# Performance work log

Measured on AMD Instinct MI355X. Metric: run time of the kernel, lower is better.

The kernel has to match this reference:

```python
import jax, jax.numpy as jnp
import numpy as np

# CogForge GroupedQueryAttention (prefill path): GQA + RoPE + sliding-window+global-token mask
B, T, DM = 2, 2048, 768
H, HKV, DH = 12, 4, 64          # d_head = d_model // n_heads
GROUPS = H // HKV               # kv_groups = 3
WIN, GLB = 512, 64              # window_size, global_tokens
THETA = 10000.0


def _rotate_half(x):
    half = x.shape[-1] // 2
    return jnp.concatenate([-x[..., half:], x[..., :half]], axis=-1)


def _rope_cos_sin(seq_len, dim, dtype):
    inv_freq = 1.0 / (THETA ** (jnp.arange(0, dim, 2, dtype=jnp.float32) / dim))
    t = jnp.arange(seq_len, dtype=jnp.float32)
    freqs = jnp.outer(t, inv_freq)                      # [T, DH/2]
    emb = jnp.concatenate([freqs, freqs], axis=-1)      # [T, DH]
    return jnp.cos(emb).astype(dtype)[None, None], jnp.sin(emb).astype(dtype)[None, None]


def _sparse_mask(seq_len):
    # allowed(i,j) = causal AND (within window OR j is a global token)
    i = jnp.arange(seq_len)[:, None]
    j = jnp.arange(seq_len)[None, :]
    allowed = (j <= i) & (((i - j) < WIN) | (j < GLB))
    return jnp.where(allowed, 0.0, -jnp.inf).astype(jnp.float32)  # [T, T]


def setup_inputs() -> dict:
    key = jax.random.key(0)
    kx, kq, kk, kv, ko = jax.random.split(key, 5)
    x = jax.random.normal(kx, (B, T, DM), jnp.float32)
    wq = jax.random.normal(kq, (DM, H * DH), jnp.float32) * 0.02
    wk = jax.random.normal(kk, (DM, HKV * DH), jnp.float32) * 0.02
    wv = jax.random.normal(kv, (DM, HKV * DH), jnp.float32) * 0.02
    wo = jax.random.normal(ko, (H * DH, DM), jnp.float32) * 0.02
    return {"x": x, "wq": wq, "wk": wk, "wv": wv, "wo": wo}


def reference(x, wq, wk, wv, wo):
    # projections -> [B, heads, T, DH]
    q = (x @ wq).reshape(B, T, H, DH).transpose(0, 2, 1, 3)
    k = (x @ wk).reshape(B, T, HKV, DH).transpose(0, 2, 1, 3)
    v = (x @ wv).reshape(B, T, HKV, DH).transpose(0, 2, 1, 3)

    cos, sin = _rope_cos_sin(T, DH, x.dtype)            # [1,1,T,DH]
    q = q * cos + _rotate_half(q) * sin
    k = k * cos + _rotate_half(k) * sin

    # expand kv heads to match query heads (GQA)
    k = jnp.repeat(k, GROUPS, axis=1)                   # [B,H,T,DH]
    v = jnp.repeat(v, GROUPS, axis=1)

    scale = 1.0 / jnp.sqrt(jnp.asarray(DH, x.dtype))
    scores = jnp.einsum('bhtd,bhsd->bhts', q, k) * scale
    scores = scores + _sparse_mask(T)[None, None]
    weights = jax.nn.softmax(scores, axis=-1)           # attn_dropout = 0.0

    out = jnp.einsum('bhts,bhsd->bhtd', weights, v)
    out = out.transpose(0, 2, 1, 3).reshape(B, T, H * DH)
    return out @ wo
```

## Files before the change

### kernel.cpp

```cpp
#include <hip/hip_runtime.h>
#include <hip/hip_bf16.h>


typedef __attribute__((ext_vector_type(8))) short bf16x8;
typedef __attribute__((ext_vector_type(4))) float f32x4;
typedef __attribute__((ext_vector_type(4))) unsigned short u16x4;

#define MFMA __builtin_amdgcn_mfma_f32_16x16x32_bf16

constexpr int BB = 2, TT = 2048, DM = 768, HH = 12, HKV = 4, DH = 64;
constexpr int WIN = 512, GLB = 64;
constexpr float SC2 = 0.18033688011112042f;

__device__ __forceinline__ unsigned short f2b(float f) {
    union { float f; unsigned int u; } v; v.f = f;
    unsigned int r = v.u + 0x7fffu + ((v.u >> 16) & 1u);
    return (unsigned short)(r >> 16);
}

#define GLOAD_LDS(gp, lp)                                                      \
    __builtin_amdgcn_global_load_lds(                                          \
        (const __attribute__((address_space(1))) void*)(gp),                   \
        (__attribute__((address_space(3))) void*)(lp), 16, 0, 0)

__global__ __launch_bounds__(256) void k_pre(const float* __restrict__ x,
                                             unsigned short* __restrict__ xb,
                                             float2* __restrict__ rope,
                                             const float* __restrict__ wq,
                                             const float* __restrict__ wk,
                                             const float* __restrict__ wv,
                                             const float* __restrict__ wo,
                                             unsigned short* __restrict__ wqT,
                                             unsigned short* __restrict__ wkT,
                                             unsigned short* __restrict__ wvT,
                                             unsigned short* __restrict__ woT) {
    __shared__ float t[32][33];
    int bid = blockIdx.x, tid = threadIdx.x;
    if (bid < 3072) {
        int i = bid * 256 + tid;
        float4 v = ((const float4*)x)[i];
        u16x4 o; o.x = f2b(v.x); o.y = f2b(v.y); o.z = f2b(v.z); o.w = f2b(v.w);
        ((u16x4*)xb)[i] = o;
        return;
    }
    if (bid < 3328) {
        int i = (bid - 3072) * 256 + tid;
        int tt = i >> 5, p = i & 31;
        float inv = exp2f(-(float)p * (13.287712379549449f / 32.0f));
        float ang = (float)tt * inv;
        rope[i] = make_float2(cosf(ang), sinf(ang));
        return;
    }
    int wb = bid - 3328;
    const float* src; unsigned short* dst; int N, tile;
    if (wb < 576)      { src = wq; dst = wqT; N = 768; tile = wb; }
    else if (wb < 768) { src = wk; dst = wkT; N = 256; tile = wb - 576; }
    else if (wb < 960) { src = wv; dst = wvT; N = 256; tile = wb - 768; }
    else               { src = wo; dst = woT; N = 768; tile = wb - 960; }
    int ntiles = N / 32;
    int k0 = (tile / ntiles) * 32, n0 = (tile % ntiles) * 32;
    int tx = tid & 31, ty = tid >> 5;
    #pragma unroll
    for (int e = 0; e < 4; ++e) {
        int r = ty + e * 8;
        t[r][tx] = src[(size_t)(k0 + r) * N + n0 + tx];
    }
    __syncthreads();
    #pragma unroll
    for (int e = 0; e < 4; ++e) {
        int r = ty + e * 8;
        dst[(size_t)(n0 + r) * DM + k0 + tx] = f2b(t[tx][r]);
    }
}

__global__ __launch_bounds__(256) void k_qkv(const unsigned short* __restrict__ xb,
                                             const unsigned short* __restrict__ wqT,
                                             const unsigned short* __restrict__ wkT,
                                             const unsigned short* __restrict__ wvT,
                                             unsigned short* __restrict__ qb,
                                             unsigned short* __restrict__ kb,
                                             unsigned short* __restrict__ vtb,
                                             const float2* __restrict__ rope) {
    __shared__ __align__(16) unsigned short Ab[2][128 * 64];
    __shared__ __align__(16) unsigned short Bb[2][64 * 64];
    const int tid = threadIdx.x;
    const int wave = tid >> 6, lane = tid & 63;
    const int quad = lane >> 4, col = lane & 15;
    const int y = blockIdx.y;
    int mode, hl;
    const unsigned short* Bt;
    if (y < 12)      { mode = 0; hl = y;      Bt = wqT + (size_t)hl * 64 * DM; }
    else if (y < 16) { mode = 1; hl = y - 12; Bt = wkT + (size_t)hl * 64 * DM; }
    else             { mode = 2; hl = y - 16; Bt = wvT + (size_t)hl * 64 * DM; }
    const int m0b = blockIdx.x * 128;

    const int rg = lane >> 3;
    const int cg = (lane & 7) ^ rg;
    const int ck = col & 7;

    f32x4 acc[2][4];
    #pragma unroll
    for (int rt = 0; rt < 2; ++rt)
        #pragma unroll
        for (int j = 0; j < 4; ++j) acc[rt][j] = f32x4{0.f, 0.f, 0.f, 0.f};

    auto stage = [&](int buf, int k) {
        #pragma unroll
        for (int m = 0; m < 4; ++m) {
            int g = wave * 4 + m;
            GLOAD_LDS(xb + (size_t)(m0b + g * 8 + rg) * DM + k + cg * 8,
                      &Ab[buf][g * 512]);
        }
        #pragma unroll
        for (int m = 0; m < 2; ++m) {
            int g = wave * 2 + m;
            GLOAD_LDS(Bt + (size_t)(g * 8 + rg) * DM + k + cg * 8,
                      &Bb[buf][g * 512]);
        }
    };

    stage(0, 0);
    __syncthreads();

    const int arow0 = (wave * 32 + col) * 64;
    const int arow1 = (wave * 32 + 16 + col) * 64;

    for (int t = 0; t < 12; ++t) {
        const int buf = t & 1;
        if (t < 11) stage(buf ^ 1, (t + 1) * 64);
        __builtin_amdgcn_s_setprio(1);
        #pragma unroll
        for (int ks = 0; ks < 2; ++ks) {
            const int p = ((ks * 4 + quad) ^ ck) * 8;
            bf16x8 a0 = *(const bf16x8*)&Ab[buf][arow0 + p];
            bf16x8 a1 = *(const bf16x8*)&Ab[buf][arow1 + p];
            #pragma unroll
            for (int j = 0; j < 4; ++j) {
                bf16x8 b = *(const bf16x8*)&Bb[buf][(j * 16 + col) * 64 + p];
                acc[0][j] = MFMA(a0, b, acc[0][j], 0, 0, 0);
                acc[1][j] = MFMA(a1, b, acc[1][j], 0, 0, 0);
            }
        }
        __builtin_amdgcn_s_setprio(0);
        __syncthreads();
    }

    if (mode == 2) {
        int b = m0b >> 11;
        #pragma unroll
        for (int j = 0; j < 4; ++j)
            #pragma unroll
            for (int rt = 0; rt < 2; ++rt)
                #pragma unroll
                for (int r = 0; r < 4; ++r) {
                    int m = m0b + wave * 32 + rt * 16 + quad * 4 + r;
                    int t = m & (TT - 1);
                    int d = j * 16 + col;
                    vtb[((size_t)(b * HKV + hl) * DH + d) * TT + t] = f2b(acc[rt][j][r]);
                }
        return;
    }
    int nheads = (mode == 0) ? HH : HKV;
    unsigned short* ob = (mode == 0) ? qb : kb;
    #pragma unroll
    for (int rt = 0; rt < 2; ++rt)
        #pragma unroll
        for (int r = 0; r < 4; ++r) {
            int m = m0b + wave * 32 + rt * 16 + quad * 4 + r;
            int t = m & (TT - 1);
            int b = m >> 11;
            float2 cs0 = rope[t * 32 + col];
            float2 cs1 = rope[t * 32 + 16 + col];
            float v0 = acc[rt][0][r], v1 = acc[rt][1][r], v2 = acc[rt][2][r], v3 = acc[rt][3][r];
            unsigned short* dst = ob + ((size_t)(b * nheads + hl) * TT + t) * DH + col;
            dst[0]  = f2b(v0 * cs0.x - v2 * cs0.y);
            dst[16] = f2b(v1 * cs1.x - v3 * cs1.y);
            dst[32] = f2b(v2 * cs0.x + v0 * cs0.y);
            dst[48] = f2b(v3 * cs1.x + v1 * cs1.y);
        }
}

__global__ __launch_bounds__(256) void k_out(const unsigned short* __restrict__ ao,
                                             const unsigned short* __restrict__ woT,
                                             float* __restrict__ out) {
    __shared__ __align__(16) unsigned short Ab[2][128 * 64];
    __shared__ __align__(16) unsigned short Bb[2][64 * 64];
    const int tid = threadIdx.x;
    const int wave = tid >> 6, lane = tid & 63;
    const int quad = lane >> 4, col = lane & 15;
    const int m0b = blockIdx.x * 128;
    const int n0 = blockIdx.y * 64;

    const int rg = lane >> 3;
    const int cg = (lane & 7) ^ rg;
    const int ck = col & 7;

    f32x4 acc[2][4];
    #pragma unroll
    for (int rt = 0; rt < 2; ++rt)
        #pragma unroll
        for (int j = 0; j < 4; ++j) acc[rt][j] = f32x4{0.f, 0.f, 0.f, 0.f};

    auto stage = [&](int buf, int k) {
        #pragma unroll
        for (int m = 0; m < 4; ++m) {
            int g = wave * 4 + m;
            GLOAD_LDS(ao + (size_t)(m0b + g * 8 + rg) * DM + k + cg * 8,
                      &Ab[buf][g * 512]);
        }
        #pragma unroll
        for (int m = 0; m < 2; ++m) {
            int g = wave * 2 + m;
            GLOAD_LDS(woT + (size_t)(n0 + g * 8 + rg) * DM + k + cg * 8,
                      &Bb[buf][g * 512]);
        }
    };

    stage(0, 0);
    __syncthreads();

    const int arow0 = (wave * 32 + col) * 64;
    const int arow1 = (wave * 32 + 16 + col) * 64;

    for (int t = 0; t < 12; ++t) {
        const int buf = t & 1;
        if (t < 11) stage(buf ^ 1, (t + 1) * 64);
        __builtin_amdgcn_s_setprio(1);
        #pragma unroll
        for (int ks = 0; ks < 2; ++ks) {
            const int p = ((ks * 4 + quad) ^ ck) * 8;
            bf16x8 a0 = *(const bf16x8*)&Ab[buf][arow0 + p];
            bf16x8 a1 = *(const bf16x8*)&Ab[buf][arow1 + p];
            #pragma unroll
            for (int j = 0; j < 4; ++j) {
                bf16x8 b = *(const bf16x8*)&Bb[buf][(j * 16 + col) * 64 + p];
                acc[0][j] = MFMA(a0, b, acc[0][j], 0, 0, 0);
                acc[1][j] = MFMA(a1, b, acc[1][j], 0, 0, 0);
            }
        }
        __builtin_amdgcn_s_setprio(0);
        __syncthreads();
    }

    #pragma unroll
    for (int rt = 0; rt < 2; ++rt)
        #pragma unroll
        for (int j = 0; j < 4; ++j)
            #pragma unroll
            for (int r = 0; r < 4; ++r) {
                int m = m0b + wave * 32 + rt * 16 + quad * 4 + r;
                out[(size_t)m * DM + n0 + j * 16 + col] = acc[rt][j][r];
            }
}

__global__ __launch_bounds__(256) void k_attn(const unsigned short* __restrict__ Q,
                                              const unsigned short* __restrict__ K,
                                              const unsigned short* __restrict__ Vt,
                                              unsigned short* __restrict__ AO) {
    __shared__ __align__(16) unsigned short kbuf[2][64 * 64];
    __shared__ __align__(16) unsigned short vbuf[2][64 * 64];
    const int lane = threadIdx.x & 63;
    const int wave = threadIdx.x >> 6;
    const int quad = lane >> 4, col = lane & 15;
    const int lbid = (blockIdx.x & 7) * 96 + (blockIdx.x >> 3);
    const int qb = lbid & 31, bh = lbid >> 5;
    const int h = bh % HH, b = bh / HH;
    const int hkv = h / 3;
    const int i0 = qb * 64 + wave * 16;
    const int irow = i0 + col;

    const unsigned short* qbase = Q + ((size_t)(b * HH + h) * TT + irow) * DH + quad * 8;
    const bf16x8 qf0 = *(const bf16x8*)qbase;
    const bf16x8 qf1 = *(const bf16x8*)(qbase + 32);
    const unsigned short* kbase = K + (size_t)(b * HKV + hkv) * TT * DH;
    const unsigned short* vbase = Vt + (size_t)(b * HKV + hkv) * DH * TT;

    float m_run = -1e30f, l_lane = 0.f;
    f32x4 accO[4];
    #pragma unroll
    for (int dt = 0; dt < 4; ++dt) accO[dt] = f32x4{0.f, 0.f, 0.f, 0.f};

    int jw0 = (qb * 64 - WIN + 1) & ~63; if (jw0 < 64) jw0 = 64;
    const int jlast = qb * 64;
    const int nt = 1 + ((jlast >= 64) ? (((jlast - jw0) >> 6) + 1) : 0);
    auto j0_of = [&](int t) { return (t == 0) ? 0 : (jw0 + ((t - 1) << 6)); };

    const int srow = wave * 16 + (lane >> 3);
    const int sk = (lane >> 3) & 7;
    const int sq = (lane & 7) ^ sk;
    const int ck = col & 7;

    const int L0 = ((((quad * 2) & 3) << 4) | col) << 2;
    const int L1 = ((((quad * 2 + 1) & 3) << 4) | col) << 2;
    const bool hiq = quad >= 2;

    uint4 g0, g1, g2, g3;
    auto stage_load = [&](int j0) {
        const unsigned short* ks = kbase + (size_t)(j0 + srow) * DH + sq * 8;
        const unsigned short* vs = vbase + (size_t)srow * TT + j0 + sq * 8;
        g0 = *(const uint4*)ks;
        g1 = *(const uint4*)(ks + 8 * DH);
        g2 = *(const uint4*)vs;
        g3 = *(const uint4*)(vs + 8 * TT);
    };
    auto stage_write = [&](int bb) {
        unsigned short* kd = &kbuf[bb][srow * 64 + (lane & 7) * 8];
        unsigned short* vd = &vbuf[bb][srow * 64 + (lane & 7) * 8];
        *(uint4*)kd = g0;
        *(uint4*)(kd + 8 * 64) = g1;
        *(uint4*)vd = g2;
        *(uint4*)(vd + 8 * 64) = g3;
    };

    stage_load(0);
    stage_write(0);
    __syncthreads();

    for (int t = 0; t < nt; ++t) {
        const int bb = t & 1;
        const bool more = (t + 1) < nt;
        if (more) stage_load(j0_of(t + 1));

        const int j0 = j0_of(t);
        const int mode = (t == 0) ? ((i0 < 64) ? 1 : 0)
                       : (((j0 + 63 > i0) || (j0 <= i0 + 15 - WIN)) ? 2 : 0);

        f32x4 sT[4];
        #pragma unroll
        for (int f = 0; f < 4; ++f) sT[f] = f32x4{0.f, 0.f, 0.f, 0.f};
        __builtin_amdgcn_s_setprio(1);
        #pragma unroll
        for (int f = 0; f < 4; ++f) {
            bf16x8 k0 = *(const bf16x8*)&kbuf[bb][(f * 16 + col) * 64 + (quad ^ ck) * 8];
            bf16x8 k1 = *(const bf16x8*)&kbuf[bb][(f * 16 + col) * 64 + ((4 + quad) ^ ck) * 8];
            sT[f] = MFMA(k0, qf0, sT[f], 0, 0, 0);
            sT[f] = MFMA(k1, qf1, sT[f], 0, 0, 0);
        }
        __builtin_amdgcn_s_setprio(0);

        const int dq = irow - j0 - quad * 4;
        if (mode == 1) {
            #pragma unroll
            for (int f = 0; f < 4; ++f)
                #pragma unroll
                for (int r = 0; r < 4; ++r)
                    if (dq - f * 16 - r < 0) sT[f][r] = -3e30f;
        } else if (mode == 2) {
            #pragma unroll
            for (int f = 0; f < 4; ++f)
                #pragma unroll
                for (int r = 0; r < 4; ++r)
                    if ((unsigned)(dq - f * 16 - r) >= (unsigned)WIN) sT[f][r] = -3e30f;
        }

        float mx = -3e30f;
        #pragma unroll
        for (int f = 0; f < 4; ++f)
            #pragma unroll
            for (int r = 0; r < 4; ++r) mx = fmaxf(mx, sT[f][r]);

        if (!__all(mx <= m_run + 44.f)) {
            float rm = fmaxf(mx, __shfl_xor(mx, 16));
            rm = fmaxf(rm, __shfl_xor(rm, 32));
            float mn = fmaxf(m_run, rm);
            float corr = exp2f((m_run - mn) * SC2);
            m_run = mn;
            l_lane *= corr;
            #pragma unroll
            for (int dt = 0; dt < 4; ++dt)
                #pragma unroll
                for (int r = 0; r < 4; ++r) accO[dt][r] *= corr;
        }

        const float mbase = m_run * SC2;
        unsigned int pk[4][2];
        float ps = 0.f;
        #pragma unroll
        for (int f = 0; f < 4; ++f) {
            float p0 = exp2f(__builtin_fmaf(sT[f][0], SC2, -mbase));
            float p1 = exp2f(__builtin_fmaf(sT[f][1], SC2, -mbase));
            float p2 = exp2f(__builtin_fmaf(sT[f][2], SC2, -mbase));
            float p3 = exp2f(__builtin_fmaf(sT[f][3], SC2, -mbase));
            ps += (p0 + p1) + (p2 + p3);
            asm("v_cvt_pk_bf16_f32 %0, %1, %2" : "=v"(pk[f][0]) : "v"(p0), "v"(p1));
            asm("v_cvt_pk_bf16_f32 %0, %1, %2" : "=v"(pk[f][1]) : "v"(p2), "v"(p3));
        }
        l_lane += ps;

        bf16x8 vf[8];
        #pragma unroll
        for (int js = 0; js < 2; ++js)
            #pragma unroll
            for (int dt = 0; dt < 4; ++dt)
                vf[js * 4 + dt] = *(const bf16x8*)
                    &vbuf[bb][(dt * 16 + col) * 64 + ((js * 4 + quad) ^ ck) * 8];

        #pragma unroll
        for (int js = 0; js < 2; ++js) {
            int fa = 2 * js, fb = 2 * js + 1;
            unsigned int a0 = __builtin_amdgcn_ds_bpermute(L0, pk[fa][0]);
            unsigned int a1 = __builtin_amdgcn_ds_bpermute(L0, pk[fa][1]);
            unsigned int a2 = __builtin_amdgcn_ds_bpermute(L1, pk[fa][0]);
            unsigned int a3 = __builtin_amdgcn_ds_bpermute(L1, pk[fa][1]);
            unsigned int b0 = __builtin_amdgcn_ds_bpermute(L0, pk[fb][0]);
            unsigned int b1 = __builtin_amdgcn_ds_bpermute(L0, pk[fb][1]);
            unsigned int b2 = __builtin_amdgcn_ds_bpermute(L1, pk[fb][0]);
            unsigned int b3 = __builtin_amdgcn_ds_bpermute(L1, pk[fb][1]);
            union { bf16x8 v; unsigned int u[4]; } pb;
            pb.u[0] = hiq ? b0 : a0;
            pb.u[1] = hiq ? b1 : a1;
            pb.u[2] = hiq ? b2 : a2;
            pb.u[3] = hiq ? b3 : a3;
            __builtin_amdgcn_s_setprio(1);
            #pragma unroll
            for (int dt = 0; dt < 4; ++dt)
                accO[dt] = MFMA(vf[js * 4 + dt], pb.v, accO[dt], 0, 0, 0);
            __builtin_amdgcn_s_setprio(0);
        }

        if (more) stage_write(bb ^ 1);
        __syncthreads();
    }

    float lr = l_lane;
    lr += __shfl_xor(lr, 16);
    lr += __shfl_xor(lr, 32);
    const float inv = 1.0f / lr;

    unsigned short* dst = AO + ((size_t)b * TT + irow) * DM + h * DH + quad * 4;
    #pragma unroll
    for (int dt = 0; dt < 4; ++dt) {
        u16x4 o;
        o.x = f2b(accO[dt][0] * inv);
        o.y = f2b(accO[dt][1] * inv);
        o.z = f2b(accO[dt][2] * inv);
        o.w = f2b(accO[dt][3] * inv);
        *(u16x4*)(dst + dt * 16) = o;
    }
}

extern "C" void kernel_launch(void* const* d_in, const int* in_sizes, int n_in,
                              void* d_out, int out_size, void* d_ws, size_t ws_size,
                              hipStream_t stream) {
    const float* x  = (const float*)d_in[0];
    const float* wq = (const float*)d_in[1];
    const float* wk = (const float*)d_in[2];
    const float* wv = (const float*)d_in[3];
    const float* wo = (const float*)d_in[4];
    float* out = (float*)d_out;

    char* ws = (char*)d_ws;
    size_t off = 0;
    auto alloc = [&](size_t bytes) -> void* {
        void* p = ws + off;
        off += (bytes + 255) & ~(size_t)255;
        return p;
    };
    const int M = BB * TT;
    unsigned short* xb  = (unsigned short*)alloc((size_t)M * DM * 2);
    unsigned short* wqT = (unsigned short*)alloc((size_t)DM * DM * 2);
    unsigned short* wkT = (unsigned short*)alloc((size_t)(HKV * DH) * DM * 2);
    unsigned short* wvT = (unsigned short*)alloc((size_t)(HKV * DH) * DM * 2);
    unsigned short* woT = (unsigned short*)alloc((size_t)DM * DM * 2);
    unsigned short* qb  = (unsigned short*)alloc((size_t)BB * HH * TT * DH * 2);
    unsigned short* kb  = (unsigned short*)alloc((size_t)BB * HKV * TT * DH * 2);
    unsigned short* vtb = (unsigned short*)alloc((size_t)BB * HKV * DH * TT * 2);
    unsigned short* ao  = (unsigned short*)alloc((size_t)M * DM * 2);
    float2* rope        = (float2*)alloc((size_t)TT * 32 * sizeof(float2));

    k_pre<<<4864, 256, 0, stream>>>(x, xb, rope, wq, wk, wv, wo, wqT, wkT, wvT, woT);
    k_qkv<<<dim3(M / 128, 20), 256, 0, stream>>>(xb, wqT, wkT, wvT, qb, kb, vtb, rope);
    k_attn<<<768, 256, 0, stream>>>(qb, kb, vtb, ao);
    k_out<<<dim3(M / 128, 12), 256, 0, stream>>>(ao, woT, out);
}
```

Measured before the change: 61.36 us.

## Give each attention wave two query tiles and stage K/V with direct-to-LDS loads

The attention kernel now runs 2 waves per block instead of 4, and each wave handles 32 query rows as two 16-row tiles. Each K and V fragment read from LDS feeds the MFMAs of both tiles, with separate softmax state per tile. K/V tile staging switches from register loads plus LDS stores to global_load_lds direct writes, issued at the top of the iteration into the other buffer. This halves LDS fragment reads per query row and removes the register round trip in staging, at the cost of more VGPRs per wave and fewer waves per block, which may lower latency hiding.

```diff
diff --git a/kernel.cpp b/kernel.cpp
--- a/kernel.cpp
+++ b/kernel.cpp
@@ -253,7 +253,7 @@
             }
 }
 
-__global__ __launch_bounds__(256) void k_attn(const unsigned short* __restrict__ Q,
+__global__ __launch_bounds__(128) void k_attn(const unsigned short* __restrict__ Q,
                                               const unsigned short* __restrict__ K,
                                               const unsigned short* __restrict__ Vt,
                                               unsigned short* __restrict__ AO) {
@@ -266,126 +266,138 @@
     const int qb = lbid & 31, bh = lbid >> 5;
     const int h = bh % HH, b = bh / HH;
     const int hkv = h / 3;
-    const int i0 = qb * 64 + wave * 16;
-    const int irow = i0 + col;
-
-    const unsigned short* qbase = Q + ((size_t)(b * HH + h) * TT + irow) * DH + quad * 8;
-    const bf16x8 qf0 = *(const bf16x8*)qbase;
-    const bf16x8 qf1 = *(const bf16x8*)(qbase + 32);
+    const int i0 = qb * 64 + wave * 32;
+    const int ir0 = i0 + col, ir1 = i0 + 16 + col;
+
+    const unsigned short* qp0 = Q + ((size_t)(b * HH + h) * TT + ir0) * DH + quad * 8;
+    const unsigned short* qp1 = Q + ((size_t)(b * HH + h) * TT + ir1) * DH + quad * 8;
+    const bf16x8 qA0 = *(const bf16x8*)qp0;
+    const bf16x8 qA1 = *(const bf16x8*)(qp0 + 32);
+    const bf16x8 qB0 = *(const bf16x8*)qp1;
+    const bf16x8 qB1 = *(const bf16x8*)(qp1 + 32);
     const unsigned short* kbase = K + (size_t)(b * HKV + hkv) * TT * DH;
     const unsigned short* vbase = Vt + (size_t)(b * HKV + hkv) * DH * TT;
 
-    float m_run = -1e30f, l_lane = 0.f;
-    f32x4 accO[4];
-    #pragma unroll
-    for (int dt = 0; dt < 4; ++dt) accO[dt] = f32x4{0.f, 0.f, 0.f, 0.f};
+    float mA = -1e30f, lA = 0.f, mB = -1e30f, lB = 0.f;
+    f32x4 oA[4], oB[4];
+    #pragma unroll
+    for (int dt = 0; dt < 4; ++dt) { oA[dt] = f32x4{0.f,0.f,0.f,0.f}; oB[dt] = f32x4{0.f,0.f,0.f,0.f}; }
 
     int jw0 = (qb * 64 - WIN + 1) & ~63; if (jw0 < 64) jw0 = 64;
     const int jlast = qb * 64;
     const int nt = 1 + ((jlast >= 64) ? (((jlast - jw0) >> 6) + 1) : 0);
     auto j0_of = [&](int t) { return (t == 0) ? 0 : (jw0 + ((t - 1) << 6)); };
 
-    const int srow = wave * 16 + (lane >> 3);
-    const int sk = (lane >> 3) & 7;
-    const int sq = (lane & 7) ^ sk;
+    const int srow = wave * 32 + (lane >> 3);
+    const int soff = ((lane & 7) ^ (lane >> 3)) * 8;
     const int ck = col & 7;
+
+    auto stage = [&](int bb, int j0) {
+        #pragma unroll
+        for (int part = 0; part < 4; ++part) {
+            GLOAD_LDS(kbase + (size_t)(j0 + srow + part * 8) * DH + soff,
+                      &kbuf[bb][(wave * 32 + part * 8) * 64]);
+            GLOAD_LDS(vbase + (size_t)(srow + part * 8) * TT + j0 + soff,
+                      &vbuf[bb][(wave * 32 + part * 8) * 64]);
+        }
+    };
 
     const int L0 = ((((quad * 2) & 3) << 4) | col) << 2;
     const int L1 = ((((quad * 2 + 1) & 3) << 4) | col) << 2;
     const bool hiq = quad >= 2;
 
-    uint4 g0, g1, g2, g3;
-    auto stage_load = [&](int j0) {
-        const unsigned short* ks = kbase + (size_t)(j0 + srow) * DH + sq * 8;
-        const unsigned short* vs = vbase + (size_t)srow * TT + j0 + sq * 8;
-        g0 = *(const uint4*)ks;
-        g1 = *(const uint4*)(ks + 8 * DH);
-        g2 = *(const uint4*)vs;
-        g3 = *(const uint4*)(vs + 8 * TT);
-    };
-    auto stage_write = [&](int bb) {
-        unsigned short* kd = &kbuf[bb][srow * 64 + (lane & 7) * 8];
-        unsigned short* vd = &vbuf[bb][srow * 64 + (lane & 7) * 8];
-        *(uint4*)kd = g0;
-        *(uint4*)(kd + 8 * 64) = g1;
-        *(uint4*)vd = g2;
-        *(uint4*)(vd + 8 * 64) = g3;
-    };
-
-    stage_load(0);
-    stage_write(0);
+    stage(0, 0);
     __syncthreads();
 
     for (int t = 0; t < nt; ++t) {
         const int bb = t & 1;
-        const bool more = (t + 1) < nt;
-        if (more) stage_load(j0_of(t + 1));
+        if (t + 1 < nt) stage(bb ^ 1, j0_of(t + 1));
 
         const int j0 = j0_of(t);
         const int mode = (t == 0) ? ((i0 < 64) ? 1 : 0)
-                       : (((j0 + 63 > i0) || (j0 <= i0 + 15 - WIN)) ? 2 : 0);
-
-        f32x4 sT[4];
-        #pragma unroll
-        for (int f = 0; f < 4; ++f) sT[f] = f32x4{0.f, 0.f, 0.f, 0.f};
+                       : (((j0 + 63 > i0) || (j0 <= i0 + 31 - WIN)) ? 2 : 0);
+
+        f32x4 sA[4], sB[4];
+        #pragma unroll
+        for (int f = 0; f < 4; ++f) { sA[f] = f32x4{0.f,0.f,0.f,0.f}; sB[f] = f32x4{0.f,0.f,0.f,0.f}; }
         __builtin_amdgcn_s_setprio(1);
         #pragma unroll
         for (int f = 0; f < 4; ++f) {
             bf16x8 k0 = *(const bf16x8*)&kbuf[bb][(f * 16 + col) * 64 + (quad ^ ck) * 8];
             bf16x8 k1 = *(const bf16x8*)&kbuf[bb][(f * 16 + col) * 64 + ((4 + quad) ^ ck) * 8];
-            sT[f] = MFMA(k0, qf0, sT[f], 0, 0, 0);
-            sT[f] = MFMA(k1, qf1, sT[f], 0, 0, 0);
+            sA[f] = MFMA(k0, qA0, sA[f], 0, 0, 0);
+            sA[f] = MFMA(k1, qA1, sA[f], 0, 0, 0);
+            sB[f] = MFMA(k0, qB0, sB[f], 0, 0, 0);
+            sB[f] = MFMA(k1, qB1, sB[f], 0, 0, 0);
         }
         __builtin_amdgcn_s_setprio(0);
 
-        const int dq = irow - j0 - quad * 4;
+        const int dqA = ir0 - j0 - quad * 4;
+        const int dqB = ir1 - j0 - quad * 4;
         if (mode == 1) {
             #pragma unroll
             for (int f = 0; f < 4; ++f)
                 #pragma unroll
-                for (int r = 0; r < 4; ++r)
-                    if (dq - f * 16 - r < 0) sT[f][r] = -3e30f;
+                for (int r = 0; r < 4; ++r) {
+                    if (dqA - f * 16 - r < 0) sA[f][r] = -3e30f;
+                    if (dqB - f * 16 - r < 0) sB[f][r] = -3e30f;
+                }
         } else if (mode == 2) {
             #pragma unroll
             for (int f = 0; f < 4; ++f)
                 #pragma unroll
-                for (int r = 0; r < 4; ++r)
-                    if ((unsigned)(dq - f * 16 - r) >= (unsigned)WIN) sT[f][r] = -3e30f;
-        }
-
-        float mx = -3e30f;
+                for (int r = 0; r < 4; ++r) {
+                    if ((unsigned)(dqA - f * 16 - r) >= (unsigned)WIN) sA[f][r] = -3e30f;
+                    if ((unsigned)(dqB - f * 16 - r) >= (unsigned)WIN) sB[f][r] = -3e30f;
+                }
+        }
+
+        float mxA = -3e30f, mxB = -3e30f;
         #pragma unroll
         for (int f = 0; f < 4; ++f)
             #pragma unroll
-            for (int r = 0; r < 4; ++r) mx = fmaxf(mx, sT[f][r]);
-
-        if (!__all(mx <= m_run + 44.f)) {
-            float rm = fmaxf(mx, __shfl_xor(mx, 16));
-            rm = fmaxf(rm, __shfl_xor(rm, 32));
-            float mn = fmaxf(m_run, rm);
-            float corr = exp2f((m_run - mn) * SC2);
-            m_run = mn;
-            l_lane *= corr;
+            for (int r = 0; r < 4; ++r) {
+                mxA = fmaxf(mxA, sA[f][r]);
+                mxB = fmaxf(mxB, sB[f][r]);
+            }
+
+        if (!__all(mxA <= mA + 44.f && mxB <= mB + 44.f)) {
+            float rA = fmaxf(mxA, __shfl_xor(mxA, 16));
+            rA = fmaxf(rA, __shfl_xor(rA, 32));
+            float rB = fmaxf(mxB, __shfl_xor(mxB, 16));
+            rB = fmaxf(rB, __shfl_xor(rB, 32));
+            float nA = fmaxf(mA, rA), nB = fmaxf(mB, rB);
+            float cA = exp2f((mA - nA) * SC2), cB = exp2f((mB - nB) * SC2);
+            mA = nA; mB = nB; lA *= cA; lB *= cB;
             #pragma unroll
             for (int dt = 0; dt < 4; ++dt)
                 #pragma unroll
-                for (int r = 0; r < 4; ++r) accO[dt][r] *= corr;
-        }
-
-        const float mbase = m_run * SC2;
-        unsigned int pk[4][2];
-        float ps = 0.f;
-        #pragma unroll
-        for (int f = 0; f < 4; ++f) {
-            float p0 = exp2f(__builtin_fmaf(sT[f][0], SC2, -mbase));
-            float p1 = exp2f(__builtin_fmaf(sT[f][1], SC2, -mbase));
-            float p2 = exp2f(__builtin_fmaf(sT[f][2], SC2, -mbase));
-            float p3 = exp2f(__builtin_fmaf(sT[f][3], SC2, -mbase));
-            ps += (p0 + p1) + (p2 + p3);
-            asm("v_cvt_pk_bf16_f32 %0, %1, %2" : "=v"(pk[f][0]) : "v"(p0), "v"(p1));
-            asm("v_cvt_pk_bf16_f32 %0, %1, %2" : "=v"(pk[f][1]) : "v"(p2), "v"(p3));
-        }
-        l_lane += ps;
+                for (int r = 0; r < 4; ++r) { oA[dt][r] *= cA; oB[dt][r] *= cB; }
+        }
+
+        unsigned int pkA[4][2], pkB[4][2];
+        {
+            const float bA = mA * SC2, bBs = mB * SC2;
+            float psA = 0.f, psB = 0.f;
+            #pragma unroll
+            for (int f = 0; f < 4; ++f) {
+                float a0 = exp2f(__builtin_fmaf(sA[f][0], SC2, -bA));
+                float a1 = exp2f(__builtin_fmaf(sA[f][1], SC2, -bA));
+                float a2 = exp2f(__builtin_fmaf(sA[f][2], SC2, -bA));
+                float a3 = exp2f(__builtin_fmaf(sA[f][3], SC2, -bA));
+                psA += (a0 + a1) + (a2 + a3);
+                asm("v_cvt_pk_bf16_f32 %0, %1, %2" : "=v"(pkA[f][0]) : "v"(a0), "v"(a1));
+                asm("v_cvt_pk_bf16_f32 %0, %1, %2" : "=v"(pkA[f][1]) : "v"(a2), "v"(a3));
+                float b0 = exp2f(__builtin_fmaf(sB[f][0], SC2, -bBs));
+                float b1 = exp2f(__builtin_fmaf(sB[f][1], SC2, -bBs));
+                float b2 = exp2f(__builtin_fmaf(sB[f][2], SC2, -bBs));
+                float b3 = exp2f(__builtin_fmaf(sB[f][3], SC2, -bBs));
+                psB += (b0 + b1) + (b2 + b3);
+                asm("v_cvt_pk_bf16_f32 %0, %1, %2" : "=v"(pkB[f][0]) : "v"(b0), "v"(b1));
+                asm("v_cvt_pk_bf16_f32 %0, %1, %2" : "=v"(pkB[f][1]) : "v"(b2), "v"(b3));
+            }
+            lA += psA; lB += psB;
+        }
 
         bf16x8 vf[8];
         #pragma unroll
@@ -398,14 +410,14 @@
         #pragma unroll
         for (int js = 0; js < 2; ++js) {
             int fa = 2 * js, fb = 2 * js + 1;
-            unsigned int a0 = __builtin_amdgcn_ds_bpermute(L0, pk[fa][0]);
-            unsigned int a1 = __builtin_amdgcn_ds_bpermute(L0, pk[fa][1]);
-            unsigned int a2 = __builtin_amdgcn_ds_bpermute(L1, pk[fa][0]);
-            unsigned int a3 = __builtin_amdgcn_ds_bpermute(L1, pk[fa][1]);
-            unsigned int b0 = __builtin_amdgcn_ds_bpermute(L0, pk[fb][0]);
-            unsigned int b1 = __builtin_amdgcn_ds_bpermute(L0, pk[fb][1]);
-            unsigned int b2 = __builtin_amdgcn_ds_bpermute(L1, pk[fb][0]);
-            unsigned int b3 = __builtin_amdgcn_ds_bpermute(L1, pk[fb][1]);
+            unsigned int a0 = __builtin_amdgcn_ds_bpermute(L0, pkA[fa][0]);
+            unsigned int a1 = __builtin_amdgcn_ds_bpermute(L0, pkA[fa][1]);
+            unsigned int a2 = __builtin_amdgcn_ds_bpermute(L1, pkA[fa][0]);
+            unsigned int a3 = __builtin_amdgcn_ds_bpermute(L1, pkA[fa][1]);
+            unsigned int b0 = __builtin_amdgcn_ds_bpermute(L0, pkA[fb][0]);
+            unsigned int b1 = __builtin_amdgcn_ds_bpermute(L0, pkA[fb][1]);
+            unsigned int b2 = __builtin_amdgcn_ds_bpermute(L1, pkA[fb][0]);
+            unsigned int b3 = __builtin_amdgcn_ds_bpermute(L1, pkA[fb][1]);
             union { bf16x8 v; unsigned int u[4]; } pb;
             pb.u[0] = hiq ? b0 : a0;
             pb.u[1] = hiq ? b1 : a1;
@@ -414,28 +426,52 @@
             __builtin_amdgcn_s_setprio(1);
             #pragma unroll
             for (int dt = 0; dt < 4; ++dt)
-                accO[dt] = MFMA(vf[js * 4 + dt], pb.v, accO[dt], 0, 0, 0);
+                oA[dt] = MFMA(vf[js * 4 + dt], pb.v, oA[dt], 0, 0, 0);
             __builtin_amdgcn_s_setprio(0);
         }
-
-        if (more) stage_write(bb ^ 1);
+        #pragma unroll
+        for (int js = 0; js < 2; ++js) {
+            int fa = 2 * js, fb = 2 * js + 1;
+            unsigned int a0 = __builtin_amdgcn_ds_bpermute(L0, pkB[fa][0]);
+            unsigned int a1 = __builtin_amdgcn_ds_bpermute(L0, pkB[fa][1]);
+            unsigned int a2 = __builtin_amdgcn_ds_bpermute(L1, pkB[fa][0]);
+            unsigned int a3 = __builtin_amdgcn_ds_bpermute(L1, pkB[fa][1]);
+            unsigned int b0 = __builtin_amdgcn_ds_bpermute(L0, pkB[fb][0]);
+            unsigned int b1 = __builtin_amdgcn_ds_bpermute(L0, pkB[fb][1]);
+            unsigned int b2 = __builtin_amdgcn_ds_bpermute(L1, pkB[fb][0]);
+            unsigned int b3 = __builtin_amdgcn_ds_bpermute(L1, pkB[fb][1]);
+            union { bf16x8 v; unsigned int u[4]; } pb;
+            pb.u[0] = hiq ? b0 : a0;
+            pb.u[1] = hiq ? b1 : a1;
+            pb.u[2] = hiq ? b2 : a2;
+            pb.u[3] = hiq ? b3 : a3;
+            __builtin_amdgcn_s_setprio(1);
+            #pragma unroll
+            for (int dt = 0; dt < 4; ++dt)
+                oB[dt] = MFMA(vf[js * 4 + dt], pb.v, oB[dt], 0, 0, 0);
+            __builtin_amdgcn_s_setprio(0);
+        }
+
         __syncthreads();
     }
 
-    float lr = l_lane;
-    lr += __shfl_xor(lr, 16);
-    lr += __shfl_xor(lr, 32);
-    const float inv = 1.0f / lr;
-
-    unsigned short* dst = AO + ((size_t)b * TT + irow) * DM + h * DH + quad * 4;
+    float lrA = lA, lrB = lB;
+    lrA += __shfl_xor(lrA, 16); lrA += __shfl_xor(lrA, 32);
+    lrB += __shfl_xor(lrB, 16); lrB += __shfl_xor(lrB, 32);
+    const float invA = 1.0f / lrA, invB = 1.0f / lrB;
+
+    unsigned short* dA = AO + ((size_t)b * TT + ir0) * DM + h * DH + quad * 4;
+    unsigned short* dB = AO + ((size_t)b * TT + ir1) * DM + h * DH + quad * 4;
     #pragma unroll
     for (int dt = 0; dt < 4; ++dt) {
         u16x4 o;
-        o.x = f2b(accO[dt][0] * inv);
-        o.y = f2b(accO[dt][1] * inv);
-        o.z = f2b(accO[dt][2] * inv);
-        o.w = f2b(accO[dt][3] * inv);
-        *(u16x4*)(dst + dt * 16) = o;
+        o.x = f2b(oA[dt][0] * invA); o.y = f2b(oA[dt][1] * invA);
+        o.z = f2b(oA[dt][2] * invA); o.w = f2b(oA[dt][3] * invA);
+        *(u16x4*)(dA + dt * 16) = o;
+        u16x4 p;
+        p.x = f2b(oB[dt][0] * invB); p.y = f2b(oB[dt][1] * invB);
+        p.z = f2b(oB[dt][2] * invB); p.w = f2b(oB[dt][3] * invB);
+        *(u16x4*)(dB + dt * 16) = p;
     }
 }
 
@@ -470,6 +506,6 @@
 
     k_pre<<<4864, 256, 0, stream>>>(x, xb, rope, wq, wk, wv, wo, wqT, wkT, wvT, woT);
     k_qkv<<<dim3(M / 128, 20), 256, 0, stream>>>(xb, wqT, wkT, wvT, qb, kb, vtb, rope);
-    k_attn<<<768, 256, 0, stream>>>(qb, kb, vtb, ao);
+    k_attn<<<768, 128, 0, stream>>>(qb, kb, vtb, ao);
     k_out<<<dim3(M / 128, 12), 256, 0, stream>>>(ao, woT, out);
 }
```

New measurement: 68.04 us. 1.11x slower.

## Stage K/V via direct global-to-LDS loads and use 16x16x16 MFMA for PV

Applied to the files above, without the earlier changes.

The K/V tile staging now uses global_load_lds directly into the double buffer, replacing the register round-trip of global loads followed by LDS stores. This frees registers and the store instructions. The PV product now uses the 16x16x16 bf16 MFMA, which consumes the packed softmax probabilities in the layout each lane already holds. That removes the ds_bpermute shuffles, at the cost of twice as many smaller MFMAs and more narrow LDS reads of V. The LDS swizzle must match the per-lane global addressing for correctness.

```diff
diff --git a/kernel.cpp b/kernel.cpp
--- a/kernel.cpp
+++ b/kernel.cpp
@@ -3,10 +3,12 @@
 
 
 typedef __attribute__((ext_vector_type(8))) short bf16x8;
+typedef __attribute__((ext_vector_type(4))) short bf16x4;
 typedef __attribute__((ext_vector_type(4))) float f32x4;
 typedef __attribute__((ext_vector_type(4))) unsigned short u16x4;
 
-#define MFMA __builtin_amdgcn_mfma_f32_16x16x32_bf16
+#define MFMA   __builtin_amdgcn_mfma_f32_16x16x32_bf16
+#define MFMA16 __builtin_amdgcn_mfma_f32_16x16x16bf16_1k
 
 constexpr int BB = 2, TT = 2048, DM = 768, HH = 12, HKV = 4, DH = 64;
 constexpr int WIN = 512, GLB = 64;
@@ -285,41 +287,27 @@
     const int nt = 1 + ((jlast >= 64) ? (((jlast - jw0) >> 6) + 1) : 0);
     auto j0_of = [&](int t) { return (t == 0) ? 0 : (jw0 + ((t - 1) << 6)); };
 
-    const int srow = wave * 16 + (lane >> 3);
-    const int sk = (lane >> 3) & 7;
-    const int sq = (lane & 7) ^ sk;
+    const int sr = lane >> 3;
+    const int soff = ((lane & 7) ^ sr) * 8;
     const int ck = col & 7;
 
-    const int L0 = ((((quad * 2) & 3) << 4) | col) << 2;
-    const int L1 = ((((quad * 2 + 1) & 3) << 4) | col) << 2;
-    const bool hiq = quad >= 2;
-
-    uint4 g0, g1, g2, g3;
-    auto stage_load = [&](int j0) {
-        const unsigned short* ks = kbase + (size_t)(j0 + srow) * DH + sq * 8;
-        const unsigned short* vs = vbase + (size_t)srow * TT + j0 + sq * 8;
-        g0 = *(const uint4*)ks;
-        g1 = *(const uint4*)(ks + 8 * DH);
-        g2 = *(const uint4*)vs;
-        g3 = *(const uint4*)(vs + 8 * TT);
+    auto stage = [&](int bb, int j0) {
+        GLOAD_LDS(kbase + (size_t)(j0 + wave * 16 + sr) * DH + soff,
+                  &kbuf[bb][(wave * 16) * 64]);
+        GLOAD_LDS(kbase + (size_t)(j0 + wave * 16 + 8 + sr) * DH + soff,
+                  &kbuf[bb][(wave * 16 + 8) * 64]);
+        GLOAD_LDS(vbase + (size_t)(wave * 16 + sr) * TT + j0 + soff,
+                  &vbuf[bb][(wave * 16) * 64]);
+        GLOAD_LDS(vbase + (size_t)(wave * 16 + 8 + sr) * TT + j0 + soff,
+                  &vbuf[bb][(wave * 16 + 8) * 64]);
     };
-    auto stage_write = [&](int bb) {
-        unsigned short* kd = &kbuf[bb][srow * 64 + (lane & 7) * 8];
-        unsigned short* vd = &vbuf[bb][srow * 64 + (lane & 7) * 8];
-        *(uint4*)kd = g0;
-        *(uint4*)(kd + 8 * 64) = g1;
-        *(uint4*)vd = g2;
-        *(uint4*)(vd + 8 * 64) = g3;
-    };
-
-    stage_load(0);
-    stage_write(0);
+
+    stage(0, 0);
     __syncthreads();
 
     for (int t = 0; t < nt; ++t) {
         const int bb = t & 1;
-        const bool more = (t + 1) < nt;
-        if (more) stage_load(j0_of(t + 1));
+        if (t + 1 < nt) stage(bb ^ 1, j0_of(t + 1));
 
         const int j0 = j0_of(t);
         const int mode = (t == 0) ? ((i0 < 64) ? 1 : 0)
@@ -387,38 +375,21 @@
         }
         l_lane += ps;
 
-        bf16x8 vf[8];
-        #pragma unroll
-        for (int js = 0; js < 2; ++js)
-            #pragma unroll
-            for (int dt = 0; dt < 4; ++dt)
-                vf[js * 4 + dt] = *(const bf16x8*)
-                    &vbuf[bb][(dt * 16 + col) * 64 + ((js * 4 + quad) ^ ck) * 8];
-
-        #pragma unroll
-        for (int js = 0; js < 2; ++js) {
-            int fa = 2 * js, fb = 2 * js + 1;
-            unsigned int a0 = __builtin_amdgcn_ds_bpermute(L0, pk[fa][0]);
-            unsigned int a1 = __builtin_amdgcn_ds_bpermute(L0, pk[fa][1]);
-            unsigned int a2 = __builtin_amdgcn_ds_bpermute(L1, pk[fa][0]);
-            unsigned int a3 = __builtin_amdgcn_ds_bpermute(L1, pk[fa][1]);
-            unsigned int b0 = __builtin_amdgcn_ds_bpermute(L0, pk[fb][0]);
-            unsigned int b1 = __builtin_amdgcn_ds_bpermute(L0, pk[fb][1]);
-            unsigned int b2 = __builtin_amdgcn_ds_bpermute(L1, pk[fb][0]);
-            unsigned int b3 = __builtin_amdgcn_ds_bpermute(L1, pk[fb][1]);
-            union { bf16x8 v; unsigned int u[4]; } pb;
-            pb.u[0] = hiq ? b0 : a0;
-            pb.u[1] = hiq ? b1 : a1;
-            pb.u[2] = hiq ? b2 : a2;
-            pb.u[3] = hiq ? b3 : a3;
-            __builtin_amdgcn_s_setprio(1);
-            #pragma unroll
-            for (int dt = 0; dt < 4; ++dt)
-                accO[dt] = MFMA(vf[js * 4 + dt], pb.v, accO[dt], 0, 0, 0);
-            __builtin_amdgcn_s_setprio(0);
-        }
-
-        if (more) stage_write(bb ^ 1);
+        __builtin_amdgcn_s_setprio(1);
+        #pragma unroll
+        for (int f = 0; f < 4; ++f) {
+            union { bf16x4 v; unsigned int u[2]; } pb;
+            pb.u[0] = pk[f][0];
+            pb.u[1] = pk[f][1];
+            const int voff = (((2 * f + (quad >> 1)) ^ ck) << 3) + ((quad & 1) << 2);
+            #pragma unroll
+            for (int dt = 0; dt < 4; ++dt) {
+                bf16x4 va = *(const bf16x4*)&vbuf[bb][(dt * 16 + col) * 64 + voff];
+                accO[dt] = MFMA16(va, pb.v, accO[dt], 0, 0, 0);
+            }
+        }
+        __builtin_amdgcn_s_setprio(0);
+
         __syncthreads();
     }
 
```

After: 61.66 us. Within noise of the previous version (+0.5%).
